# Kernel tuning notes

Hardware: AMD Instinct MI355X
Metric: run time of the kernel (lower is better)

Reference implementation:

```python
import jax, jax.numpy as jnp
import numpy as np

B, NX, NC, D, H = 2, 512, 4096, 1024, 16
HD = D // H  # head_dim = context_dim // heads
LN_EPS = 1e-5


def setup_inputs() -> dict:
    key = jax.random.key(0)
    k0, k1, k2, k3, k4 = jax.random.split(key, 5)
    x = jax.random.normal(k0, (B, NX, D), dtype=jnp.float32)
    c = jax.random.normal(k1, (B, NC, D), dtype=jnp.float32)
    attn_mask = jax.random.randint(k2, (B, NX, NC), 0, 2).astype(bool)
    # learned params
    ln_w = jnp.ones((D,), jnp.float32)
    ln_b = jnp.zeros((D,), jnp.float32)
    Wq = jax.random.normal(k3, (D, D), dtype=jnp.float32) * 0.02  # to_q (query_dim -> inner_dim)
    Wo = jax.random.normal(k4, (D, D), dtype=jnp.float32) * 0.02  # to_out (inner_dim -> query_dim)
    return {"x": x, "c": c, "attn_mask": attn_mask, "ln_w": ln_w, "ln_b": ln_b, "Wq": Wq, "Wo": Wo}


def _layernorm(x, w, b):
    mu = jnp.mean(x, axis=-1, keepdims=True)
    var = jnp.mean(jnp.square(x - mu), axis=-1, keepdims=True)
    return (x - mu) * jax.lax.rsqrt(var + LN_EPS) * w + b


def reference(x, c, attn_mask, ln_w, ln_b, Wq, Wo):
    scale = HD ** (-0.5)
    xn = _layernorm(x, ln_w, ln_b)
    q = (xn @ Wq).reshape(B, NX, H, HD).transpose(0, 2, 1, 3)      # (B,H,NX,HD)
    kv0 = c.reshape(B, NC, H, HD).transpose(0, 2, 1, 3)             # (B,H,NC,HD) -- kvt=(kv0,kv0)
    kv = jnp.concatenate([q, kv0], axis=2)                          # kv_append_q=True -> (B,H,NX+NC,HD)
    # mask: ones for the appended-q block, user mask for context block
    m = jnp.broadcast_to(attn_mask[:, None, :, :], (B, H, NX, NC))
    full_mask = jnp.concatenate([jnp.ones((B, H, NX, NX), bool), m], axis=-1)
    sim = jnp.einsum('bhqd,bhkd->bhqk', q * scale, kv)              # (B,H,NX,NX+NC)
    neg = -jnp.finfo(sim.dtype).max
    sim = jnp.where(full_mask, sim, neg)
    attn = jax.nn.softmax(sim, axis=-1)
    a = jnp.einsum('bhqk,bhkd->bhqd', attn, kv)
    o = a.transpose(0, 2, 1, 3).reshape(B, NX, H * HD) @ Wo
    return (o, kv0)
```

## Files before the change

### kernel.cpp

```cpp
#include <hip/hip_runtime.h>

#define B_  2
#define NX_ 512
#define NC_ 4096
#define D_  1024
#define H_  16
#define HD_ 64
#define NT_ (NX_ + NC_)
#define NSPLIT 6
#define KBS (NT_ / 64 / NSPLIT)

typedef float  floatx4  __attribute__((ext_vector_type(4)));
typedef __bf16 bf16x8   __attribute__((ext_vector_type(8)));
typedef unsigned short ushort8v __attribute__((ext_vector_type(8)));

__device__ __forceinline__ bf16x8 as_bf16x8(ushort8v u) {
    union { ushort8v u; bf16x8 b; } c; c.u = u; return c.b;
}
__device__ __forceinline__ unsigned short f2bf(float f) {
    unsigned u = __float_as_uint(f);
    u += 0x7FFF + ((u >> 16) & 1);
    return (unsigned short)(u >> 16);
}

__global__ __launch_bounds__(256)
void prep_kernel(const float* __restrict__ x, const float* __restrict__ lw,
                 const float* __restrict__ lb, const float* __restrict__ Wq,
                 const float* __restrict__ Wo, const int* __restrict__ mask,
                 const float* __restrict__ c,
                 unsigned short* __restrict__ xnb, unsigned short* __restrict__ WqT,
                 unsigned short* __restrict__ WoT, unsigned* __restrict__ bits,
                 unsigned short* __restrict__ cbf, float* __restrict__ gz,
                 float* __restrict__ kv0o) {
    int blk = blockIdx.x;
    int tid = threadIdx.x;
    if (blk < 1024) {
        int row = blk;
        float4 v = reinterpret_cast<const float4*>(x)[(size_t)row * (D_ / 4) + tid];
        float s  = v.x + v.y + v.z + v.w;
        float s2 = v.x * v.x + v.y * v.y + v.z * v.z + v.w * v.w;
        #pragma unroll
        for (int off = 32; off > 0; off >>= 1) {
            s  += __shfl_down(s, off);
            s2 += __shfl_down(s2, off);
        }
        __shared__ float sm[4], sm2[4], stat[2];
        int wv = tid >> 6;
        if ((tid & 63) == 0) { sm[wv] = s; sm2[wv] = s2; }
        __syncthreads();
        if (tid == 0) {
            float S  = sm[0] + sm[1] + sm[2] + sm[3];
            float S2 = sm2[0] + sm2[1] + sm2[2] + sm2[3];
            float mu  = S * (1.0f / D_);
            float var = fmaxf(S2 * (1.0f / D_) - mu * mu, 0.0f);
            stat[0] = mu;
            stat[1] = rsqrtf(var + 1e-5f);
        }
        __syncthreads();
        float mu = stat[0], rs = stat[1];
        float4 w4 = reinterpret_cast<const float4*>(lw)[tid];
        float4 b4 = reinterpret_cast<const float4*>(lb)[tid];
        ushort4 o;
        o.x = f2bf((v.x - mu) * rs * w4.x + b4.x);
        o.y = f2bf((v.y - mu) * rs * w4.y + b4.y);
        o.z = f2bf((v.z - mu) * rs * w4.z + b4.z);
        o.w = f2bf((v.w - mu) * rs * w4.w + b4.w);
        reinterpret_cast<ushort4*>(xnb)[(size_t)row * (D_ / 4) + tid] = o;
    } else if (blk < 1536) {
        int which = (blk - 1024) >> 8;
        int t = (blk - 1024) & 255;
        const float* W = which ? Wo : Wq;
        unsigned short* WT = which ? WoT : WqT;
        __shared__ unsigned short T[64][72];
        int row0 = (t >> 4) * 64, col0 = (t & 15) * 64;
        int r = tid >> 2, ch = (tid & 3) * 16;
        const float* src = W + (size_t)(row0 + r) * D_ + col0 + ch;
        unsigned short vals[16];
        #pragma unroll
        for (int k = 0; k < 4; ++k) {
            float4 v = reinterpret_cast<const float4*>(src)[k];
            vals[k*4+0] = f2bf(v.x); vals[k*4+1] = f2bf(v.y);
            vals[k*4+2] = f2bf(v.z); vals[k*4+3] = f2bf(v.w);
        }
        #pragma unroll
        for (int i = 0; i < 16; ++i) T[ch + i][r] = vals[i];
        __syncthreads();
        unsigned short* dst = WT + (size_t)(col0 + r) * D_ + row0 + ch;
        uint4 o0 = *reinterpret_cast<uint4*>(&T[r][ch]);
        uint4 o1 = *reinterpret_cast<uint4*>(&T[r][ch + 8]);
        *reinterpret_cast<uint4*>(dst)     = o0;
        *reinterpret_cast<uint4*>(dst + 8) = o1;
    } else if (blk < 2048) {
        size_t w = (size_t)(blk - 1536) * 256 + tid;
        const int* src = mask + w * 32;
        unsigned b = 0;
        #pragma unroll
        for (int k = 0; k < 8; ++k) {
            int4 v = reinterpret_cast<const int4*>(src)[k];
            b |= (v.x != 0 ? 1u : 0u) << (k * 4 + 0);
            b |= (v.y != 0 ? 1u : 0u) << (k * 4 + 1);
            b |= (v.z != 0 ? 1u : 0u) << (k * 4 + 2);
            b |= (v.w != 0 ? 1u : 0u) << (k * 4 + 3);
        }
        bits[w] = b;
    } else if (blk < 10240) {
        size_t i = ((size_t)(blk - 2048) * 256 + tid) * 4;
        float4 v = *reinterpret_cast<const float4*>(c + i);
        ushort4 o;
        o.x = f2bf(v.x); o.y = f2bf(v.y); o.z = f2bf(v.z); o.w = f2bf(v.w);
        *reinterpret_cast<ushort4*>(cbf + i) = o;
        if (kv0o != nullptr) {
            size_t row = i >> 10;
            int dd = (int)(i & 1023);
            int hh = dd >> 6, d4 = (dd & 63) >> 2;
            int bb = (int)(row >> 12);
            int n  = (int)(row & 4095);
            size_t o4 = (((size_t)(bb * 16 + hh) * NC_ + n) << 4) + d4;
            reinterpret_cast<float4*>(kv0o)[o4] = v;
        }
    } else {
        size_t i = ((size_t)(blk - 10240) * 256 + tid) * 4;
        float4 z = {0.f, 0.f, 0.f, 0.f};
        *reinterpret_cast<float4*>(gz + i) = z;
    }
}

__global__ __launch_bounds__(256)
void kv0_kernel(const float* __restrict__ c, float* __restrict__ out2) {
    size_t i = (size_t)blockIdx.x * 256 + threadIdx.x;
    int d4 = (int)(i & 15);
    size_t r = i >> 4;
    int n = (int)(r % NC_);
    size_t r2 = r / NC_;
    int h = (int)(r2 & (H_ - 1));
    int b = (int)(r2 >> 4);
    float4 v = *reinterpret_cast<const float4*>(c + ((size_t)(b * NC_ + n)) * D_ + h * HD_ + d4 * 4);
    reinterpret_cast<float4*>(out2)[i] = v;
}

__global__ __launch_bounds__(256)
void gemm_bt_kernel(const unsigned short* __restrict__ A, const unsigned short* __restrict__ BT,
                    unsigned short* __restrict__ Cb) {
    __shared__ unsigned short As[64][72];
    __shared__ unsigned short Bs[64][72];
    int tid = threadIdx.x;
    int lane = tid & 63, wave = tid >> 6;
    int m16 = lane & 15, g = lane >> 4, g8 = g * 8;
    int row0 = blockIdx.y * 64, col0 = blockIdx.x * 64;
    int r = tid >> 2, ch = (tid & 3) * 16;

    floatx4 acc[4];
    #pragma unroll
    for (int t = 0; t < 4; ++t) acc[t] = (floatx4){0.f, 0.f, 0.f, 0.f};

    for (int kc = 0; kc < 16; ++kc) {
        int k0 = kc * 64;
        const unsigned short* asrc = A  + (size_t)(row0 + r) * D_ + k0 + ch;
        const unsigned short* bsrc = BT + (size_t)(col0 + r) * D_ + k0 + ch;
        uint4 a0 = *reinterpret_cast<const uint4*>(asrc);
        uint4 a1 = *reinterpret_cast<const uint4*>(asrc + 8);
        uint4 b0 = *reinterpret_cast<const uint4*>(bsrc);
        uint4 b1 = *reinterpret_cast<const uint4*>(bsrc + 8);
        *reinterpret_cast<uint4*>(&As[r][ch])     = a0;
        *reinterpret_cast<uint4*>(&As[r][ch + 8]) = a1;
        *reinterpret_cast<uint4*>(&Bs[r][ch])     = b0;
        *reinterpret_cast<uint4*>(&Bs[r][ch + 8]) = b1;
        __syncthreads();
        bf16x8 fa0 = as_bf16x8(*reinterpret_cast<ushort8v*>(&As[16 * wave + m16][g8]));
        bf16x8 fa1 = as_bf16x8(*reinterpret_cast<ushort8v*>(&As[16 * wave + m16][32 + g8]));
        #pragma unroll
        for (int t = 0; t < 4; ++t) {
            bf16x8 fb0 = as_bf16x8(*reinterpret_cast<ushort8v*>(&Bs[16 * t + m16][g8]));
            bf16x8 fb1 = as_bf16x8(*reinterpret_cast<ushort8v*>(&Bs[16 * t + m16][32 + g8]));
            acc[t] = __builtin_amdgcn_mfma_f32_16x16x32_bf16(fa0, fb0, acc[t], 0, 0, 0);
            acc[t] = __builtin_amdgcn_mfma_f32_16x16x32_bf16(fa1, fb1, acc[t], 0, 0, 0);
        }
        __syncthreads();
    }
    #pragma unroll
    for (int t = 0; t < 4; ++t)
        #pragma unroll
        for (int reg = 0; reg < 4; ++reg)
            Cb[(size_t)(row0 + 16 * wave + g * 4 + reg) * D_ + col0 + 16 * t + m16] = f2bf(acc[t][reg]);
}

__global__ __launch_bounds__(256)
void gemm_attn_kernel(const float* __restrict__ gacc, const float* __restrict__ gacc_l,
                      const unsigned short* __restrict__ BT, float* __restrict__ out) {
    __shared__ unsigned short As[64][72];
    __shared__ unsigned short Bs[64][72];
    int tid = threadIdx.x;
    int lane = tid & 63, wave = tid >> 6;
    int m16 = lane & 15, g = lane >> 4, g8 = g * 8;
    int row0 = blockIdx.y * 64, col0 = blockIdx.x * 64;
    int r = tid >> 2, ch = (tid & 3) * 16;

    floatx4 acc[4];
    #pragma unroll
    for (int t = 0; t < 4; ++t) acc[t] = (floatx4){0.f, 0.f, 0.f, 0.f};

    for (int kc = 0; kc < 16; ++kc) {
        int k0 = kc * 64;
        int row = row0 + r;
        float inv = 1.0f / fmaxf(gacc_l[(size_t)row * H_ + kc], 1e-35f);
        const float* asrc = gacc + (size_t)row * D_ + k0 + ch;
        const unsigned short* bsrc = BT + (size_t)(col0 + r) * D_ + k0 + ch;
        unsigned short av[16];
        #pragma unroll
        for (int t = 0; t < 4; ++t) {
            float4 v = reinterpret_cast<const float4*>(asrc)[t];
            av[t*4+0] = f2bf(v.x * inv); av[t*4+1] = f2bf(v.y * inv);
            av[t*4+2] = f2bf(v.z * inv); av[t*4+3] = f2bf(v.w * inv);
        }
        uint4 b0 = *reinterpret_cast<const uint4*>(bsrc);
        uint4 b1 = *reinterpret_cast<const uint4*>(bsrc + 8);
        *reinterpret_cast<uint4*>(&As[r][ch])     = *reinterpret_cast<uint4*>(&av[0]);
        *reinterpret_cast<uint4*>(&As[r][ch + 8]) = *reinterpret_cast<uint4*>(&av[8]);
        *reinterpret_cast<uint4*>(&Bs[r][ch])     = b0;
        *reinterpret_cast<uint4*>(&Bs[r][ch + 8]) = b1;
        __syncthreads();
        bf16x8 fa0 = as_bf16x8(*reinterpret_cast<ushort8v*>(&As[16 * wave + m16][g8]));
        bf16x8 fa1 = as_bf16x8(*reinterpret_cast<ushort8v*>(&As[16 * wave + m16][32 + g8]));
        #pragma unroll
        for (int t = 0; t < 4; ++t) {
            bf16x8 fb0 = as_bf16x8(*reinterpret_cast<ushort8v*>(&Bs[16 * t + m16][g8]));
            bf16x8 fb1 = as_bf16x8(*reinterpret_cast<ushort8v*>(&Bs[16 * t + m16][32 + g8]));
            acc[t] = __builtin_amdgcn_mfma_f32_16x16x32_bf16(fa0, fb0, acc[t], 0, 0, 0);
            acc[t] = __builtin_amdgcn_mfma_f32_16x16x32_bf16(fa1, fb1, acc[t], 0, 0, 0);
        }
        __syncthreads();
    }
    #pragma unroll
    for (int t = 0; t < 4; ++t)
        #pragma unroll
        for (int reg = 0; reg < 4; ++reg)
            out[(size_t)(row0 + 16 * wave + g * 4 + reg) * D_ + col0 + 16 * t + m16] = acc[t][reg];
}

__global__ __launch_bounds__(256, 6)
void attn_kernel(const unsigned short* __restrict__ qbf,
                 const unsigned short* __restrict__ cbf,
                 const unsigned* __restrict__ maskbits,
                 float* __restrict__ gacc, float* __restrict__ gacc_l) {
    int blk   = blockIdx.x;
    int xcd   = blk & 7;
    int rest  = blk >> 3;
    int grp   = rest / 48;
    int inner = rest - grp * 48;
    int bh    = grp * 8 + xcd;
    int qt    = inner & 7;
    int split = inner >> 3;
    int h  = bh & 15;
    int b  = bh >> 4;
    int tid  = threadIdx.x;
    int lane = tid & 63;
    int wave = tid >> 6;
    int m16  = lane & 15;
    int g    = lane >> 4;
    int g8   = g * 8;

    __shared__ unsigned short Ks [64][72];
    __shared__ unsigned short Kts[64][72];
    __shared__ unsigned short Ps [64][64];

    const unsigned short* qrow = qbf + ((size_t)(b * NX_ + qt * 64 + 16 * wave + m16)) * D_ + h * HD_;
    bf16x8 qa0 = as_bf16x8(*reinterpret_cast<const ushort8v*>(qrow + g8));
    bf16x8 qa1 = as_bf16x8(*reinterpret_cast<const ushort8v*>(qrow + 32 + g8));

    floatx4 acc_o[4];
    #pragma unroll
    for (int td = 0; td < 4; ++td) acc_o[td] = (floatx4){0.f, 0.f, 0.f, 0.f};
    floatx4 acc_l = (floatx4){0.f, 0.f, 0.f, 0.f};

    ushort8v ones_u;
    #pragma unroll
    for (int j = 0; j < 8; ++j) ones_u[j] = 0x3F80;
    bf16x8 onesf = as_bf16x8(ones_u);

    int Kg = tid >> 4;
    int Dg = tid & 15;
    int pcst = ((Kg >> 1) + (Dg >> 1)) & 7;
    int prsw = 2 * ((m16 >> 2) & 3);

    int kb0 = split * KBS;

    uint2 rows[4];
    {
        const unsigned short* s0 = (kb0 < 8)
            ? qbf + ((size_t)(b * NX_ + kb0 * 64 + 4 * Kg)) * D_ + h * HD_ + 4 * Dg
            : cbf + ((size_t)(b * NC_ + kb0 * 64 - NX_ + 4 * Kg)) * D_ + h * HD_ + 4 * Dg;
        #pragma unroll
        for (int kk = 0; kk < 4; ++kk)
            rows[kk] = *reinterpret_cast<const uint2*>(s0 + (size_t)kk * D_);
    }

    for (int i = 0; i < KBS; ++i) {
        int kb = kb0 + i;
        __syncthreads();

        unsigned mw0[4], mw1[4];
        if (kb >= 8) {
            #pragma unroll
            for (int r = 0; r < 4; ++r) {
                size_t mi = ((size_t)(b * NX_ + qt * 64 + 16 * wave + g * 4 + r)) * (NC_ / 32)
                          + (size_t)(kb - 8) * 2;
                uint2 w = *reinterpret_cast<const uint2*>(&maskbits[mi]);
                mw0[r] = w.x; mw1[r] = w.y;
            }
        }

        #pragma unroll
        for (int kk = 0; kk < 4; ++kk)
            *reinterpret_cast<uint2*>(&Ks[4 * Kg + kk][4 * Dg]) = rows[kk];
        #pragma unroll
        for (int i2 = 0; i2 < 4; ++i2) {
            unsigned sel = (i2 & 1) ? 0x07060302u : 0x05040100u;
            unsigned r0 = (i2 >> 1) ? rows[0].y : rows[0].x;
            unsigned r1 = (i2 >> 1) ? rows[1].y : rows[1].x;
            unsigned r2 = (i2 >> 1) ? rows[2].y : rows[2].x;
            unsigned r3 = (i2 >> 1) ? rows[3].y : rows[3].x;
            uint2 cw;
            cw.x = __builtin_amdgcn_perm(r1, r0, sel);
            cw.y = __builtin_amdgcn_perm(r3, r2, sel);
            *reinterpret_cast<uint2*>(&Kts[4 * Dg + i2][pcst * 8 + 4 * (Kg & 1)]) = cw;
        }

        {
            int kbn = (i + 1 < KBS) ? kb + 1 : kb;
            const unsigned short* sn = (kbn < 8)
                ? qbf + ((size_t)(b * NX_ + kbn * 64 + 4 * Kg)) * D_ + h * HD_ + 4 * Dg
                : cbf + ((size_t)(b * NC_ + kbn * 64 - NX_ + 4 * Kg)) * D_ + h * HD_ + 4 * Dg;
            #pragma unroll
            for (int kk = 0; kk < 4; ++kk)
                rows[kk] = *reinterpret_cast<const uint2*>(sn + (size_t)kk * D_);
        }

        asm volatile("s_waitcnt lgkmcnt(0)" ::: "memory");
        __builtin_amdgcn_s_barrier();
        __builtin_amdgcn_sched_barrier(0);
        asm volatile("" ::: "memory");

        floatx4 accs[4];
        #pragma unroll
        for (int t = 0; t < 4; ++t) {
            bf16x8 b0 = as_bf16x8(*reinterpret_cast<ushort8v*>(&Ks[16 * t + m16][g8]));
            bf16x8 b1 = as_bf16x8(*reinterpret_cast<ushort8v*>(&Ks[16 * t + m16][32 + g8]));
            floatx4 d = (floatx4){0.f, 0.f, 0.f, 0.f};
            d = __builtin_amdgcn_mfma_f32_16x16x32_bf16(qa0, b0, d, 0, 0, 0);
            d = __builtin_amdgcn_mfma_f32_16x16x32_bf16(qa1, b1, d, 0, 0, 0);
            accs[t] = d;
        }

        const float C1 = 0.18033688011112042f;
        const float C2 = 92.33248261689366f;
        #pragma unroll
        for (int t = 0; t < 4; ++t) {
            int cc = 2 * t + (m16 >> 3);
            #pragma unroll
            for (int r = 0; r < 4; ++r) {
                float e = fminf(fmaf(accs[t][r], C1, -C2), 0.0f);
                float p = __builtin_amdgcn_exp2f(e);
                if (kb >= 8) {
                    unsigned w = (t < 2) ? mw0[r] : mw1[r];
                    unsigned bit = (w >> ((16 * t + m16) & 31)) & 1u;
                    p = bit ? p : 0.0f;
                }
                int prow = 16 * wave + g * 4 + r;
                int pc = (cc + 2 * g) & 7;
                Ps[prow][pc * 8 + (m16 & 7)] = (unsigned short)(__float_as_uint(p) >> 16);
            }
        }
        asm volatile("s_waitcnt lgkmcnt(0)" ::: "memory");

        bf16x8 p0 = as_bf16x8(*reinterpret_cast<ushort8v*>(&Ps[16 * wave + m16][((g + prsw) & 7) * 8]));
        bf16x8 p1 = as_bf16x8(*reinterpret_cast<ushort8v*>(&Ps[16 * wave + m16][((4 + g + prsw) & 7) * 8]));
        acc_l = __builtin_amdgcn_mfma_f32_16x16x32_bf16(p0, onesf, acc_l, 0, 0, 0);
        acc_l = __builtin_amdgcn_mfma_f32_16x16x32_bf16(p1, onesf, acc_l, 0, 0, 0);
        #pragma unroll
        for (int td = 0; td < 4; ++td) {
            int row = 16 * td + m16;
            int rh = row >> 3;
            bf16x8 v0 = as_bf16x8(*reinterpret_cast<ushort8v*>(&Kts[row][((g + rh) & 7) * 8]));
            bf16x8 v1 = as_bf16x8(*reinterpret_cast<ushort8v*>(&Kts[row][((4 + g + rh) & 7) * 8]));
            acc_o[td] = __builtin_amdgcn_mfma_f32_16x16x32_bf16(p0, v0, acc_o[td], 0, 0, 0);
            acc_o[td] = __builtin_amdgcn_mfma_f32_16x16x32_bf16(p1, v1, acc_o[td], 0, 0, 0);
        }
    }

    #pragma unroll
    for (int r = 0; r < 4; ++r) {
        int qrow_ = qt * 64 + 16 * wave + g * 4 + r;
        float* dst = gacc + ((size_t)(b * NX_ + qrow_)) * D_ + h * HD_;
        #pragma unroll
        for (int td = 0; td < 4; ++td)
            unsafeAtomicAdd(&dst[16 * td + m16], acc_o[td][r]);
        if (m16 == 0)
            unsafeAtomicAdd(&gacc_l[(size_t)(b * NX_ + qrow_) * H_ + h], acc_l[r]);
    }
}

extern "C" void kernel_launch(void* const* d_in, const int* in_sizes, int n_in,
                              void* d_out, int out_size, void* d_ws, size_t ws_size,
                              hipStream_t stream) {
    (void)in_sizes; (void)n_in; (void)out_size;
    const float* x    = (const float*)d_in[0];
    const float* c    = (const float*)d_in[1];
    const int*   mask = (const int*)d_in[2];
    const float* ln_w = (const float*)d_in[3];
    const float* ln_b = (const float*)d_in[4];
    const float* Wq   = (const float*)d_in[5];
    const float* Wo   = (const float*)d_in[6];
    float* out  = (float*)d_out;
    float* out2 = out + (size_t)B_ * NX_ * D_;

    const size_t SCRATCH_FLOATS = 8011776;
    bool use_ws = (d_ws != nullptr) && (ws_size >= SCRATCH_FLOATS * sizeof(float));
    float* base = use_ws ? (float*)d_ws : out2;

    unsigned short* qbf      = (unsigned short*)(base);
    unsigned*       maskbits = (unsigned*)(base + 524288);
    float*          gacc     = base + 655360;
    float*          gacc_l   = base + 1703936;
    unsigned short* WqT      = (unsigned short*)(base + 1720320);
    unsigned short* WoT      = (unsigned short*)(base + 2244608);
    unsigned short* xnb      = (unsigned short*)(base + 2768896);
    unsigned short* cbf      = (unsigned short*)(base + 3817472);

    prep_kernel<<<11280, 256, 0, stream>>>(x, ln_w, ln_b, Wq, Wo, mask, c,
                                           xnb, WqT, WoT, maskbits, cbf, gacc,
                                           use_ws ? out2 : nullptr);
    gemm_bt_kernel<<<dim3(16, 16), 256, 0, stream>>>(xnb, WqT, qbf);
    attn_kernel<<<NSPLIT * 256, 256, 0, stream>>>(qbf, cbf, maskbits, gacc, gacc_l);
    gemm_attn_kernel<<<dim3(16, 16), 256, 0, stream>>>(gacc, gacc_l, WoT, out);
    if (!use_ws)
        kv0_kernel<<<(B_ * H_ * NC_ * HD_ / 4) / 256, 256, 0, stream>>>(c, out2);
}
```

Measured before the change: 223.3 us.

## Drop LDS staging in projection GEMMs and reduce attention split count to four

Both projection GEMMs (Q projection and output projection) now load MFMA operands straight from global memory into registers. This removes the shared-memory tiles and barriers, uses a 64x32 output tile, and doubles the grid. The attention kernel's key split drops from 6 to 4, with occupancy bounds and block-index decoding changed to match. The aim is to remove sync and LDS overhead in the small GEMMs and cut partial-result traffic in attention, at the cost of redundant global loads and fewer blocks to fill the GPU during attention.

```diff
diff --git a/kernel.cpp b/kernel.cpp
--- a/kernel.cpp
+++ b/kernel.cpp
@@ -7,7 +7,7 @@
 #define H_  16
 #define HD_ 64
 #define NT_ (NX_ + NC_)
-#define NSPLIT 6
+#define NSPLIT 4
 #define KBS (NT_ / 64 / NSPLIT)
 
 typedef float  floatx4  __attribute__((ext_vector_type(4)));
@@ -21,6 +21,12 @@
     unsigned u = __float_as_uint(f);
     u += 0x7FFF + ((u >> 16) & 1);
     return (unsigned short)(u >> 16);
+}
+__device__ __forceinline__ bf16x8 cvt8(float4 a, float4 b, float s) {
+    ushort8v u;
+    u[0] = f2bf(a.x * s); u[1] = f2bf(a.y * s); u[2] = f2bf(a.z * s); u[3] = f2bf(a.w * s);
+    u[4] = f2bf(b.x * s); u[5] = f2bf(b.y * s); u[6] = f2bf(b.z * s); u[7] = f2bf(b.w * s);
+    return as_bf16x8(u);
 }
 
 __global__ __launch_bounds__(256)
@@ -141,113 +147,92 @@
 __global__ __launch_bounds__(256)
 void gemm_bt_kernel(const unsigned short* __restrict__ A, const unsigned short* __restrict__ BT,
                     unsigned short* __restrict__ Cb) {
-    __shared__ unsigned short As[64][72];
-    __shared__ unsigned short Bs[64][72];
     int tid = threadIdx.x;
     int lane = tid & 63, wave = tid >> 6;
     int m16 = lane & 15, g = lane >> 4, g8 = g * 8;
-    int row0 = blockIdx.y * 64, col0 = blockIdx.x * 64;
-    int r = tid >> 2, ch = (tid & 3) * 16;
-
-    floatx4 acc[4];
-    #pragma unroll
-    for (int t = 0; t < 4; ++t) acc[t] = (floatx4){0.f, 0.f, 0.f, 0.f};
-
+    int row0 = blockIdx.y * 64, col0 = blockIdx.x * 32;
+
+    const unsigned short* arow  = A  + (size_t)(row0 + 16 * wave + m16) * D_ + g8;
+    const unsigned short* brow0 = BT + (size_t)(col0 + m16)            * D_ + g8;
+    const unsigned short* brow1 = BT + (size_t)(col0 + 16 + m16)       * D_ + g8;
+
+    floatx4 acc0 = (floatx4){0.f, 0.f, 0.f, 0.f};
+    floatx4 acc1 = (floatx4){0.f, 0.f, 0.f, 0.f};
+
+    #pragma unroll 4
     for (int kc = 0; kc < 16; ++kc) {
         int k0 = kc * 64;
-        const unsigned short* asrc = A  + (size_t)(row0 + r) * D_ + k0 + ch;
-        const unsigned short* bsrc = BT + (size_t)(col0 + r) * D_ + k0 + ch;
-        uint4 a0 = *reinterpret_cast<const uint4*>(asrc);
-        uint4 a1 = *reinterpret_cast<const uint4*>(asrc + 8);
-        uint4 b0 = *reinterpret_cast<const uint4*>(bsrc);
-        uint4 b1 = *reinterpret_cast<const uint4*>(bsrc + 8);
-        *reinterpret_cast<uint4*>(&As[r][ch])     = a0;
-        *reinterpret_cast<uint4*>(&As[r][ch + 8]) = a1;
-        *reinterpret_cast<uint4*>(&Bs[r][ch])     = b0;
-        *reinterpret_cast<uint4*>(&Bs[r][ch + 8]) = b1;
-        __syncthreads();
-        bf16x8 fa0 = as_bf16x8(*reinterpret_cast<ushort8v*>(&As[16 * wave + m16][g8]));
-        bf16x8 fa1 = as_bf16x8(*reinterpret_cast<ushort8v*>(&As[16 * wave + m16][32 + g8]));
-        #pragma unroll
-        for (int t = 0; t < 4; ++t) {
-            bf16x8 fb0 = as_bf16x8(*reinterpret_cast<ushort8v*>(&Bs[16 * t + m16][g8]));
-            bf16x8 fb1 = as_bf16x8(*reinterpret_cast<ushort8v*>(&Bs[16 * t + m16][32 + g8]));
-            acc[t] = __builtin_amdgcn_mfma_f32_16x16x32_bf16(fa0, fb0, acc[t], 0, 0, 0);
-            acc[t] = __builtin_amdgcn_mfma_f32_16x16x32_bf16(fa1, fb1, acc[t], 0, 0, 0);
-        }
-        __syncthreads();
+        bf16x8 fa0 = as_bf16x8(*reinterpret_cast<const ushort8v*>(arow  + k0));
+        bf16x8 fa1 = as_bf16x8(*reinterpret_cast<const ushort8v*>(arow  + k0 + 32));
+        bf16x8 f00 = as_bf16x8(*reinterpret_cast<const ushort8v*>(brow0 + k0));
+        bf16x8 f01 = as_bf16x8(*reinterpret_cast<const ushort8v*>(brow0 + k0 + 32));
+        bf16x8 f10 = as_bf16x8(*reinterpret_cast<const ushort8v*>(brow1 + k0));
+        bf16x8 f11 = as_bf16x8(*reinterpret_cast<const ushort8v*>(brow1 + k0 + 32));
+        acc0 = __builtin_amdgcn_mfma_f32_16x16x32_bf16(fa0, f00, acc0, 0, 0, 0);
+        acc0 = __builtin_amdgcn_mfma_f32_16x16x32_bf16(fa1, f01, acc0, 0, 0, 0);
+        acc1 = __builtin_amdgcn_mfma_f32_16x16x32_bf16(fa0, f10, acc1, 0, 0, 0);
+        acc1 = __builtin_amdgcn_mfma_f32_16x16x32_bf16(fa1, f11, acc1, 0, 0, 0);
     }
     #pragma unroll
-    for (int t = 0; t < 4; ++t)
-        #pragma unroll
-        for (int reg = 0; reg < 4; ++reg)
-            Cb[(size_t)(row0 + 16 * wave + g * 4 + reg) * D_ + col0 + 16 * t + m16] = f2bf(acc[t][reg]);
+    for (int reg = 0; reg < 4; ++reg) {
+        size_t rr = (size_t)(row0 + 16 * wave + g * 4 + reg) * D_ + col0;
+        Cb[rr + m16]      = f2bf(acc0[reg]);
+        Cb[rr + 16 + m16] = f2bf(acc1[reg]);
+    }
 }
 
 __global__ __launch_bounds__(256)
 void gemm_attn_kernel(const float* __restrict__ gacc, const float* __restrict__ gacc_l,
                       const unsigned short* __restrict__ BT, float* __restrict__ out) {
-    __shared__ unsigned short As[64][72];
-    __shared__ unsigned short Bs[64][72];
     int tid = threadIdx.x;
     int lane = tid & 63, wave = tid >> 6;
     int m16 = lane & 15, g = lane >> 4, g8 = g * 8;
-    int row0 = blockIdx.y * 64, col0 = blockIdx.x * 64;
-    int r = tid >> 2, ch = (tid & 3) * 16;
-
-    floatx4 acc[4];
-    #pragma unroll
-    for (int t = 0; t < 4; ++t) acc[t] = (floatx4){0.f, 0.f, 0.f, 0.f};
-
+    int row0 = blockIdx.y * 64, col0 = blockIdx.x * 32;
+    int row = row0 + 16 * wave + m16;
+
+    const float* arow = gacc + (size_t)row * D_ + g8;
+    const float* lrow = gacc_l + (size_t)row * H_;
+    const unsigned short* brow0 = BT + (size_t)(col0 + m16)      * D_ + g8;
+    const unsigned short* brow1 = BT + (size_t)(col0 + 16 + m16) * D_ + g8;
+
+    floatx4 acc0 = (floatx4){0.f, 0.f, 0.f, 0.f};
+    floatx4 acc1 = (floatx4){0.f, 0.f, 0.f, 0.f};
+
+    #pragma unroll 4
     for (int kc = 0; kc < 16; ++kc) {
         int k0 = kc * 64;
-        int row = row0 + r;
-        float inv = 1.0f / fmaxf(gacc_l[(size_t)row * H_ + kc], 1e-35f);
-        const float* asrc = gacc + (size_t)row * D_ + k0 + ch;
-        const unsigned short* bsrc = BT + (size_t)(col0 + r) * D_ + k0 + ch;
-        unsigned short av[16];
-        #pragma unroll
-        for (int t = 0; t < 4; ++t) {
-            float4 v = reinterpret_cast<const float4*>(asrc)[t];
-            av[t*4+0] = f2bf(v.x * inv); av[t*4+1] = f2bf(v.y * inv);
-            av[t*4+2] = f2bf(v.z * inv); av[t*4+3] = f2bf(v.w * inv);
-        }
-        uint4 b0 = *reinterpret_cast<const uint4*>(bsrc);
-        uint4 b1 = *reinterpret_cast<const uint4*>(bsrc + 8);
-        *reinterpret_cast<uint4*>(&As[r][ch])     = *reinterpret_cast<uint4*>(&av[0]);
-        *reinterpret_cast<uint4*>(&As[r][ch + 8]) = *reinterpret_cast<uint4*>(&av[8]);
-        *reinterpret_cast<uint4*>(&Bs[r][ch])     = b0;
-        *reinterpret_cast<uint4*>(&Bs[r][ch + 8]) = b1;
-        __syncthreads();
-        bf16x8 fa0 = as_bf16x8(*reinterpret_cast<ushort8v*>(&As[16 * wave + m16][g8]));
-        bf16x8 fa1 = as_bf16x8(*reinterpret_cast<ushort8v*>(&As[16 * wave + m16][32 + g8]));
-        #pragma unroll
-        for (int t = 0; t < 4; ++t) {
-            bf16x8 fb0 = as_bf16x8(*reinterpret_cast<ushort8v*>(&Bs[16 * t + m16][g8]));
-            bf16x8 fb1 = as_bf16x8(*reinterpret_cast<ushort8v*>(&Bs[16 * t + m16][32 + g8]));
-            acc[t] = __builtin_amdgcn_mfma_f32_16x16x32_bf16(fa0, fb0, acc[t], 0, 0, 0);
-            acc[t] = __builtin_amdgcn_mfma_f32_16x16x32_bf16(fa1, fb1, acc[t], 0, 0, 0);
-        }
-        __syncthreads();
+        float inv = 1.0f / fmaxf(lrow[kc], 1e-35f);
+        float4 a0 = *reinterpret_cast<const float4*>(arow + k0);
+        float4 a1 = *reinterpret_cast<const float4*>(arow + k0 + 4);
+        float4 a2 = *reinterpret_cast<const float4*>(arow + k0 + 32);
+        float4 a3 = *reinterpret_cast<const float4*>(arow + k0 + 36);
+        bf16x8 fa0 = cvt8(a0, a1, inv);
+        bf16x8 fa1 = cvt8(a2, a3, inv);
+        bf16x8 f00 = as_bf16x8(*reinterpret_cast<const ushort8v*>(brow0 + k0));
+        bf16x8 f01 = as_bf16x8(*reinterpret_cast<const ushort8v*>(brow0 + k0 + 32));
+        bf16x8 f10 = as_bf16x8(*reinterpret_cast<const ushort8v*>(brow1 + k0));
+        bf16x8 f11 = as_bf16x8(*reinterpret_cast<const ushort8v*>(brow1 + k0 + 32));
+        acc0 = __builtin_amdgcn_mfma_f32_16x16x32_bf16(fa0, f00, acc0, 0, 0, 0);
+        acc0 = __builtin_amdgcn_mfma_f32_16x16x32_bf16(fa1, f01, acc0, 0, 0, 0);
+        acc1 = __builtin_amdgcn_mfma_f32_16x16x32_bf16(fa0, f10, acc1, 0, 0, 0);
+        acc1 = __builtin_amdgcn_mfma_f32_16x16x32_bf16(fa1, f11, acc1, 0, 0, 0);
     }
     #pragma unroll
-    for (int t = 0; t < 4; ++t)
-        #pragma unroll
-        for (int reg = 0; reg < 4; ++reg)
-            out[(size_t)(row0 + 16 * wave + g * 4 + reg) * D_ + col0 + 16 * t + m16] = acc[t][reg];
-}
-
-__global__ __launch_bounds__(256, 6)
+    for (int reg = 0; reg < 4; ++reg) {
+        size_t rr = (size_t)(row0 + 16 * wave + g * 4 + reg) * D_ + col0;
+        out[rr + m16]      = acc0[reg];
+        out[rr + 16 + m16] = acc1[reg];
+    }
+}
+
+__global__ __launch_bounds__(256, 4)
 void attn_kernel(const unsigned short* __restrict__ qbf,
                  const unsigned short* __restrict__ cbf,
                  const unsigned* __restrict__ maskbits,
                  float* __restrict__ gacc, float* __restrict__ gacc_l) {
     int blk   = blockIdx.x;
-    int xcd   = blk & 7;
-    int rest  = blk >> 3;
-    int grp   = rest / 48;
-    int inner = rest - grp * 48;
-    int bh    = grp * 8 + xcd;
+    int bh    = ((blk >> 8) << 3) | (blk & 7);
+    int inner = (blk >> 3) & 31;
     int qt    = inner & 7;
     int split = inner >> 3;
     int h  = bh & 15;
@@ -429,9 +414,9 @@
     prep_kernel<<<11280, 256, 0, stream>>>(x, ln_w, ln_b, Wq, Wo, mask, c,
                                            xnb, WqT, WoT, maskbits, cbf, gacc,
                                            use_ws ? out2 : nullptr);
-    gemm_bt_kernel<<<dim3(16, 16), 256, 0, stream>>>(xnb, WqT, qbf);
+    gemm_bt_kernel<<<dim3(32, 16), 256, 0, stream>>>(xnb, WqT, qbf);
     attn_kernel<<<NSPLIT * 256, 256, 0, stream>>>(qbf, cbf, maskbits, gacc, gacc_l);
-    gemm_attn_kernel<<<dim3(16, 16), 256, 0, stream>>>(gacc, gacc_l, WoT, out);
+    gemm_attn_kernel<<<dim3(32, 16), 256, 0, stream>>>(gacc, gacc_l, WoT, out);
     if (!use_ws)
         kv0_kernel<<<(B_ * H_ * NC_ * HD_ / 4) / 256, 256, 0, stream>>>(c, out2);
 }
```

New measurement: 213.8 us. 1.04x faster.
